# Kernel tuning notes

Hardware: AMD Instinct MI355X
Metric: run time of the kernel (lower is better)

## Reference

```python
import jax, jax.numpy as jnp
import numpy as np

EPS = 1e-9
NEG_BIG = -(2.0**32) + 1.0


def dice(x, alpha):
    # BN with center=False, scale=False at inference: moving_mean=0, moving_var=1
    x_norm = x * (1.0 / np.sqrt(1.0 + EPS)).astype(np.float32)
    p = jax.nn.sigmoid(x_norm)
    return alpha * (1.0 - p) * x + p * x


def setup_inputs() -> dict:
    key = jax.random.key(0)
    ks = jax.random.split(key, 12)
    B, T, D = 4096, 200, 128
    U = 128  # gru units == hidden_dim

    def glorot(k, shape):
        fan_in = shape[0]
        return (jax.random.normal(k, shape, dtype=jnp.float32) / np.sqrt(fan_in)).astype(jnp.float32)

    return {
        "interest_seq": jax.random.normal(ks[0], (B, T, D), dtype=jnp.float32),
        "target_emb": jax.random.normal(ks[1], (B, D), dtype=jnp.float32),
        "seq_length": jax.random.randint(ks[2], (B, 1), 0, T, dtype=jnp.int32),
        "W_att1": glorot(ks[3], (4 * D, 64)),
        "alpha1": jnp.zeros((64,), jnp.float32),
        "W_att2": glorot(ks[4], (64, 16)),
        "alpha2": jnp.zeros((16,), jnp.float32),
        "W_att3": glorot(ks[5], (16, 1)),
        "W_u": glorot(ks[6], (D + U, U)),
        "W_r": glorot(ks[7], (D + U, U)),
        "W_c": glorot(ks[8], (D + U, U)),
    }


def reference(interest_seq, target_emb, seq_length, W_att1, alpha1, W_att2, alpha2, W_att3, W_u, W_r, W_c):
    B, T, D = interest_seq.shape
    U = W_u.shape[1]

    # ---- Attention scores (return_score=True, sigmoid, no weight norm) ----
    q = jnp.broadcast_to(target_emb[:, None, :], (B, T, D))  # [B,T,D]
    k = interest_seq
    att_in = jnp.concatenate([q, k, q - k, q * k], axis=-1)  # [B,T,4D]
    h1 = dice(jnp.einsum('btf,fh->bth', att_in, W_att1), alpha1)
    h2 = dice(jnp.einsum('bth,hg->btg', h1, W_att2), alpha2)
    score = jnp.einsum('btg,go->bto', h2, W_att3)  # [B,T,1]

    valid = jnp.arange(T)[None, :] < seq_length  # [B,T] bool
    vmask = valid.astype(jnp.float32)[:, :, None]
    score = score * vmask + (1.0 - vmask) * NEG_BIG
    att = jax.nn.sigmoid(score)[:, :, 0]  # [B,T]

    # ---- AUGRU scan (return final hidden state) ----
    def step(h, xs):
        x_t, a_t, m_t = xs  # [B,D], [B], [B] bool
        gi = jnp.concatenate([x_t, h], axis=-1)  # [B, D+U]
        u = jax.nn.sigmoid(gi @ W_u)
        r = jax.nn.sigmoid(gi @ W_r)
        c = jnp.tanh(jnp.concatenate([x_t, r * h], axis=-1) @ W_c)
        u_t = u * a_t[:, None]
        h_new = (1.0 - u_t) * h + u_t * c
        h = jnp.where(m_t[:, None], h_new, h)
        return h, None

    xs = (jnp.swapaxes(interest_seq, 0, 1),  # [T,B,D]
          att.T,                              # [T,B]
          valid.T)                            # [T,B]
    h0 = jnp.zeros((B, U), dtype=interest_seq.dtype)
    h_final, _ = jax.lax.scan(step, h0, xs)
    return h_final
```

## Files before the change

kernel.cpp:

```cpp
#include <hip/hip_runtime.h>
#include <math.h>

typedef __bf16 bf16;
typedef __bf16 bf16x8 __attribute__((ext_vector_type(8)));
typedef float  f32x4  __attribute__((ext_vector_type(4)));

#define MFMA16(a,b,c) __builtin_amdgcn_mfma_f32_16x16x32_bf16((a),(b),(c),0,0,0)

#define B_SZ 4096
#define T_SZ 200
#define D_SZ 128
#define U_SZ 128
#define ACHUNK 4
#define AROWS 16

__device__ __forceinline__ float frcp_(float x) { return __builtin_amdgcn_rcpf(x); }
__device__ __forceinline__ float fsig(float x)  { return frcp_(1.0f + __expf(-x)); }
__device__ __forceinline__ float ftanh_(float x){ return 1.0f - 2.0f * frcp_(1.0f + __expf(2.0f * x)); }
__device__ __forceinline__ float dicef(float x, float alpha) {
    float p = fsig(x);
    return alpha * (1.0f - p) * x + p * x;
}
__device__ __forceinline__ void bar_lgkm() {
    asm volatile("s_waitcnt lgkmcnt(0)\n\ts_barrier" ::: "memory");
}

__global__ __launch_bounds__(256) void prep_kernel(
    const float* __restrict__ Q,
    const float* __restrict__ W1,
    const float* __restrict__ W2,
    float* __restrict__ BIAS,
    bf16*  __restrict__ W1P,
    bf16*  __restrict__ W2T)
{
    const int tid = threadIdx.x;
    if (blockIdx.x == 256) {
        #pragma unroll 4
        for (int it = 0; it < 64; ++it) {
            int idx = it * 256 + tid;
            int k = idx >> 6;
            int n = idx & 63;
            float v;
            if (k < 128) v = W1[(128 + k) * 64 + n] - W1[(256 + k) * 64 + n];
            else         v = W1[(384 + (k - 128)) * 64 + n];
            W1P[n * 256 + k] = (bf16)v;
        }
        #pragma unroll
        for (int it = 0; it < 4; ++it) {
            int idx = it * 256 + tid; int k = idx >> 4; int n = idx & 15;
            W2T[n * 64 + k] = (bf16)W2[k * 16 + n];
        }
        return;
    }
    const int b0   = blockIdx.x * 16;
    const int lane = tid & 63;
    const int w    = tid >> 6;
    const int quad = lane >> 4;
    const int l15  = lane & 15;

    bf16x8 a[4];
    #pragma unroll
    for (int kk = 0; kk < 4; ++kk) {
        const float* p = Q + (long)(b0 + l15) * D_SZ + kk * 32 + quad * 8;
        float4 x0 = ((const float4*)p)[0];
        float4 x1 = ((const float4*)p)[1];
        float xv[8] = {x0.x, x0.y, x0.z, x0.w, x1.x, x1.y, x1.z, x1.w};
        #pragma unroll
        for (int j = 0; j < 8; ++j) a[kk][j] = (bf16)xv[j];
    }
    const int n = w * 16 + l15;
    f32x4 acc = {};
    #pragma unroll
    for (int kk = 0; kk < 4; ++kk) {
        bf16x8 bf;
        #pragma unroll
        for (int j = 0; j < 8; ++j) {
            int k = kk * 32 + quad * 8 + j;
            bf[j] = (bf16)(W1[k * 64 + n] + W1[(256 + k) * 64 + n]);
        }
        acc = MFMA16(a[kk], bf, acc);
    }
    #pragma unroll
    for (int i = 0; i < 4; ++i)
        BIAS[(long)(b0 + quad * 4 + i) * 64 + n] = acc[i];
}

__global__ __launch_bounds__(512) void fused_kernel(
    const float* __restrict__ X,
    const float* __restrict__ Q,
    const int*   __restrict__ LEN,
    const float* __restrict__ A1,
    const float* __restrict__ A2g,
    const float* __restrict__ W3g,
    const float* __restrict__ BIAS,
    const bf16*  __restrict__ W1P,
    const bf16*  __restrict__ W2T,
    const float* __restrict__ WU,
    const float* __restrict__ WR,
    const float* __restrict__ WC,
    float* __restrict__ OUT)
{
    __shared__ bf16  Xs[2][ACHUNK][16][136];
    __shared__ bf16  XQs[ACHUNK][16][136];
    __shared__ bf16  W1s[64 * 264];
    __shared__ bf16  Hb[16][136];
    __shared__ bf16  RHb[16][136];
    __shared__ bf16  H1s[ACHUNK * 16 * 72];
    __shared__ float qf[16 * 132];
    __shared__ float bias_s[16 * 68];
    __shared__ float As[ACHUNK * 16];
    __shared__ int   lens16[16];

    const int tid  = threadIdx.x;
    const int lane = tid & 63;
    const int w    = tid >> 6;
    const int quad = lane >> 4;
    const int l15  = lane & 15;
    const int b0   = blockIdx.x * AROWS;
    const int n    = w * 16 + l15;

    for (int idx = tid; idx < 64 * 32; idx += 512) {
        int nn = idx >> 5, k8 = idx & 31;
        *(bf16x8*)&W1s[nn * 264 + k8 * 8] = *(const bf16x8*)(W1P + nn * 256 + k8 * 8);
    }
    for (int i = tid; i < 16 * 128; i += 512) {
        int r = i >> 7, k = i & 127;
        qf[r * 132 + k] = Q[(long)(b0 + r) * D_SZ + k];
    }
    for (int i = tid; i < 16 * 64; i += 512) {
        int r = i >> 6, c2 = i & 63;
        bias_s[r * 68 + c2] = BIAS[(long)(b0 + r) * 64 + c2];
    }
    if (tid < 16) lens16[tid] = LEN[b0 + tid];
    for (int i = tid; i < 16 * 136; i += 512) { ((bf16*)Hb)[i] = (bf16)0.f; ((bf16*)RHb)[i] = (bf16)0.f; }

    const float al1v = A1[(w & 3) * 16 + l15];
    const float al2v = A2g[l15];
    const float w3v  = W3g[l15];
    bf16x8 b2f[2];
    #pragma unroll
    for (int kk = 0; kk < 2; ++kk)
        b2f[kk] = *(const bf16x8*)(W2T + l15 * 64 + kk * 32 + quad * 8);

    bf16x8 Wf[3][2][4];
    {
        const float* Wg[3] = {WU, WR, WC};
        #pragma unroll
        for (int g = 0; g < 3; ++g)
            #pragma unroll
            for (int p = 0; p < 2; ++p)
                #pragma unroll
                for (int kk = 0; kk < 4; ++kk) {
                    #pragma unroll
                    for (int i = 0; i < 8; ++i) {
                        int k = p * 128 + kk * 32 + quad * 8 + i;
                        Wf[g][p][kk][i] = (bf16)Wg[g][k * 128 + n];
                    }
                }
    }

    float h[4] = {0.f, 0.f, 0.f, 0.f};

    float4 pf[4];
    auto issue_loads = [&](int c) {
        #pragma unroll
        for (int it = 0; it < 4; ++it) {
            int gidx = it * 512 + tid;
            int c4 = gidx & 31;
            int pair = gidx >> 5;
            int r = pair & 15;
            int s = pair >> 4;
            pf[it] = *(const float4*)(X + ((long)(b0 + r) * T_SZ + (c * ACHUNK + s)) * D_SZ + c4 * 4);
        }
    };
    auto commit_part = [&](int bufw, int it) {
        int gidx = it * 512 + tid;
        int c4 = gidx & 31;
        int pair = gidx >> 5;
        int r = pair & 15;
        int sl = pair >> 4;
        float4 v = pf[it];
        float4 qv = *(const float4*)&qf[r * 132 + c4 * 4];
        bf16* dx = &Xs[bufw][sl][r][c4 * 4];
        bf16* dq = &XQs[sl][r][c4 * 4];
        dx[0] = (bf16)v.x; dx[1] = (bf16)v.y; dx[2] = (bf16)v.z; dx[3] = (bf16)v.w;
        dq[0] = (bf16)(v.x * qv.x); dq[1] = (bf16)(v.y * qv.y);
        dq[2] = (bf16)(v.z * qv.z); dq[3] = (bf16)(v.w * qv.w);
    };
    auto xparts = [&](int bufw, int s, f32x4& pr_, f32x4& pu_, f32x4& pc_) {
        f32x4 r0 = {}, u0 = {}, c0 = {};
        #pragma unroll
        for (int kk = 0; kk < 4; ++kk) {
            bf16x8 ax = *(const bf16x8*)&Xs[bufw][s][l15][kk * 32 + quad * 8];
            r0 = MFMA16(ax, Wf[1][0][kk], r0);
            u0 = MFMA16(ax, Wf[0][0][kk], u0);
            c0 = MFMA16(ax, Wf[2][0][kk], c0);
        }
        pr_ = r0; pu_ = u0; pc_ = c0;
    };
    auto h1f = [&](int bufw, int s) {
        f32x4 acc = {};
        #pragma unroll
        for (int kk = 0; kk < 4; ++kk) {
            bf16x8 ax = *(const bf16x8*)&Xs[bufw][s][l15][kk * 32 + quad * 8];
            bf16x8 bw = *(const bf16x8*)&W1s[n * 264 + kk * 32 + quad * 8];
            acc = MFMA16(ax, bw, acc);
        }
        #pragma unroll
        for (int kk = 0; kk < 4; ++kk) {
            bf16x8 aq = *(const bf16x8*)&XQs[s][l15][kk * 32 + quad * 8];
            bf16x8 bw = *(const bf16x8*)&W1s[n * 264 + 128 + kk * 32 + quad * 8];
            acc = MFMA16(aq, bw, acc);
        }
        #pragma unroll
        for (int i = 0; i < 4; ++i) {
            int row = quad * 4 + i;
            float v = acc[i] + bias_s[row * 68 + n];
            H1s[(s * 16 + row) * 72 + n] = (bf16)dicef(v, al1v);
        }
    };
    auto h23f = [&](int s, int cc) {
        f32x4 acc2 = {};
        #pragma unroll
        for (int kk = 0; kk < 2; ++kk) {
            bf16x8 a2 = *(const bf16x8*)&H1s[(s * 16 + l15) * 72 + kk * 32 + quad * 8];
            acc2 = MFMA16(a2, b2f[kk], acc2);
        }
        float sv[4];
        #pragma unroll
        for (int i = 0; i < 4; ++i) sv[i] = dicef(acc2[i], al2v) * w3v;
        #pragma unroll
        for (int i = 0; i < 4; ++i) {
            sv[i] += __shfl_xor(sv[i], 1, 64);
            sv[i] += __shfl_xor(sv[i], 2, 64);
            sv[i] += __shfl_xor(sv[i], 4, 64);
            sv[i] += __shfl_xor(sv[i], 8, 64);
        }
        if (l15 == 0) {
            int t = cc * ACHUNK + s;
            #pragma unroll
            for (int i = 0; i < 4; ++i) {
                int row = quad * 4 + i;
                As[s * 16 + row] = (t < lens16[row]) ? fsig(sv[i]) : 0.0f;
            }
        }
    };

    issue_loads(0);
    __syncthreads();
    #pragma unroll
    for (int it = 0; it < 4; ++it) commit_part(0, it);
    bar_lgkm();
    if (w < 4) { h1f(0, 0); h1f(0, 1); h1f(0, 2); h1f(0, 3); }
    bar_lgkm();

    f32x4 pr, pu, pc;
    xparts(0, 0, pr, pu, pc);

    const int NCH = T_SZ / ACHUNK;
    for (int c = 0; c < NCH; ++c) {
        const int buf  = c & 1;
        const int bufN = buf ^ 1;
        if (c + 1 < NCH) issue_loads(c + 1);

        #pragma unroll
        for (int s = 0; s < ACHUNK; ++s) {
            bf16x8 ah[4];
            #pragma unroll
            for (int kk = 0; kk < 4; ++kk)
                ah[kk] = *(const bf16x8*)&Hb[l15][kk * 32 + quad * 8];
            #pragma unroll
            for (int kk = 0; kk < 4; ++kk) {
                pr = MFMA16(ah[kk], Wf[1][1][kk], pr);
                pu = MFMA16(ah[kk], Wf[0][1][kk], pu);
            }
            float uu[4];
            #pragma unroll
            for (int i = 0; i < 4; ++i) {
                float rr = fsig(pr[i]);
                RHb[quad * 4 + i][n] = (bf16)(rr * h[i]);
                uu[i] = fsig(pu[i]);
            }
            if (w >= 4) {
                if (w == 4 + s) h23f(s, c);
            } else if (s >= 1 && c + 1 < NCH) {
                h1f(bufN, s - 1);
            }
            bar_lgkm();
            bf16x8 ar[4];
            #pragma unroll
            for (int kk = 0; kk < 4; ++kk)
                ar[kk] = *(const bf16x8*)&RHb[l15][kk * 32 + quad * 8];
            #pragma unroll
            for (int kk = 0; kk < 4; ++kk)
                pc = MFMA16(ar[kk], Wf[2][1][kk], pc);
            f32x4 prN, puN, pcN;
            if (s + 1 < ACHUNK) xparts(buf, s + 1, prN, puN, pcN);
            #pragma unroll
            for (int i = 0; i < 4; ++i) {
                float a  = As[s * 16 + quad * 4 + i];
                float cg = ftanh_(pc[i]);
                float ut = uu[i] * a;
                float hn = (1.f - ut) * h[i] + ut * cg;
                h[i] = hn;
                Hb[quad * 4 + i][n] = (bf16)hn;
            }
            if (c + 1 < NCH) commit_part(bufN, s);
            bar_lgkm();
            if (s + 1 < ACHUNK) { pr = prN; pu = puN; pc = pcN; }
        }
        if (c + 1 < NCH) {
            xparts(bufN, 0, pr, pu, pc);
            if (w < 4) h1f(bufN, 3);
        }
    }

    #pragma unroll
    for (int i = 0; i < 4; ++i)
        OUT[(long)(b0 + quad * 4 + i) * U_SZ + n] = h[i];
}

extern "C" void kernel_launch(void* const* d_in, const int* in_sizes, int n_in,
                              void* d_out, int out_size, void* d_ws, size_t ws_size,
                              hipStream_t stream) {
    const float* X   = (const float*)d_in[0];
    const float* Q   = (const float*)d_in[1];
    const int*   LEN = (const int*)d_in[2];
    const float* W1  = (const float*)d_in[3];
    const float* A1  = (const float*)d_in[4];
    const float* W2  = (const float*)d_in[5];
    const float* A2  = (const float*)d_in[6];
    const float* W3  = (const float*)d_in[7];
    const float* WU  = (const float*)d_in[8];
    const float* WR  = (const float*)d_in[9];
    const float* WC  = (const float*)d_in[10];
    float* OUT = (float*)d_out;

    float* BIAS = (float*)d_ws;
    bf16*  W1P  = (bf16*)(BIAS + (size_t)B_SZ * 64);
    bf16*  W2T  = W1P + 64 * 256;

    prep_kernel<<<257, 256, 0, stream>>>(Q, W1, W2, BIAS, W1P, W2T);
    fused_kernel<<<B_SZ / AROWS, 512, 0, stream>>>(X, Q, LEN, A1, A2, W3,
                                                   BIAS, W1P, W2T, WU, WR, WC, OUT);
}
```

Measured before the change: 809.8 us.

## Split fused kernel into GRU waves and dedicated attention producer waves

The block grows from 8 to 12 waves. Eight waves run only the AUGRU recurrence. Four producer waves load X, convert it to bf16, compute the attention MLP and write scores into double-buffered As, staying in barrier lockstep with the GRU steps. The XQ shared buffer is dropped because producers keep x and x*q in registers, and s_setprio is raised around the MFMA sections. The aim is to take attention and load work off the recurrence critical path, at the cost of more registers per wave (launch bounds 768,3) and tight barrier coupling.

```diff
diff --git a/kernel.cpp b/kernel.cpp
--- a/kernel.cpp
+++ b/kernel.cpp
@@ -13,6 +13,7 @@
 #define U_SZ 128
 #define ACHUNK 4
 #define AROWS 16
+#define NCH (T_SZ / ACHUNK)
 
 __device__ __forceinline__ float frcp_(float x) { return __builtin_amdgcn_rcpf(x); }
 __device__ __forceinline__ float fsig(float x)  { return frcp_(1.0f + __expf(-x)); }
@@ -85,7 +86,7 @@
         BIAS[(long)(b0 + quad * 4 + i) * 64 + n] = acc[i];
 }
 
-__global__ __launch_bounds__(512) void fused_kernel(
+__global__ __launch_bounds__(768, 3) void fused_kernel(
     const float* __restrict__ X,
     const float* __restrict__ Q,
     const int*   __restrict__ LEN,
@@ -101,14 +102,13 @@
     float* __restrict__ OUT)
 {
     __shared__ bf16  Xs[2][ACHUNK][16][136];
-    __shared__ bf16  XQs[ACHUNK][16][136];
-    __shared__ bf16  W1s[64 * 264];
     __shared__ bf16  Hb[16][136];
     __shared__ bf16  RHb[16][136];
-    __shared__ bf16  H1s[ACHUNK * 16 * 72];
-    __shared__ float qf[16 * 132];
-    __shared__ float bias_s[16 * 68];
-    __shared__ float As[ACHUNK * 16];
+    __shared__ bf16  H1p[4][16][72];
+    __shared__ bf16  W1s[64][264];
+    __shared__ float qf[16][132];
+    __shared__ float bias_s[16][68];
+    __shared__ float As[2][64];
     __shared__ int   lens16[16];
 
     const int tid  = threadIdx.x;
@@ -117,207 +117,229 @@
     const int quad = lane >> 4;
     const int l15  = lane & 15;
     const int b0   = blockIdx.x * AROWS;
-    const int n    = w * 16 + l15;
-
-    for (int idx = tid; idx < 64 * 32; idx += 512) {
+
+    for (int idx = tid; idx < 64 * 32; idx += 768) {
         int nn = idx >> 5, k8 = idx & 31;
-        *(bf16x8*)&W1s[nn * 264 + k8 * 8] = *(const bf16x8*)(W1P + nn * 256 + k8 * 8);
-    }
-    for (int i = tid; i < 16 * 128; i += 512) {
+        *(bf16x8*)&W1s[nn][k8 * 8] = *(const bf16x8*)(W1P + nn * 256 + k8 * 8);
+    }
+    for (int i = tid; i < 16 * 128; i += 768) {
         int r = i >> 7, k = i & 127;
-        qf[r * 132 + k] = Q[(long)(b0 + r) * D_SZ + k];
-    }
-    for (int i = tid; i < 16 * 64; i += 512) {
-        int r = i >> 6, c2 = i & 63;
-        bias_s[r * 68 + c2] = BIAS[(long)(b0 + r) * 64 + c2];
+        qf[r][k] = Q[(long)(b0 + r) * D_SZ + k];
+    }
+    for (int i = tid; i < 16 * 64; i += 768) {
+        int r = i >> 6, cc = i & 63;
+        bias_s[r][cc] = BIAS[(long)(b0 + r) * 64 + cc];
     }
     if (tid < 16) lens16[tid] = LEN[b0 + tid];
-    for (int i = tid; i < 16 * 136; i += 512) { ((bf16*)Hb)[i] = (bf16)0.f; ((bf16*)RHb)[i] = (bf16)0.f; }
-
-    const float al1v = A1[(w & 3) * 16 + l15];
-    const float al2v = A2g[l15];
-    const float w3v  = W3g[l15];
-    bf16x8 b2f[2];
-    #pragma unroll
-    for (int kk = 0; kk < 2; ++kk)
-        b2f[kk] = *(const bf16x8*)(W2T + l15 * 64 + kk * 32 + quad * 8);
-
-    bf16x8 Wf[3][2][4];
-    {
-        const float* Wg[3] = {WU, WR, WC};
-        #pragma unroll
-        for (int g = 0; g < 3; ++g)
-            #pragma unroll
-            for (int p = 0; p < 2; ++p)
+    for (int i = tid; i < 16 * 136; i += 768) {
+        ((bf16*)Hb)[i] = (bf16)0.f; ((bf16*)RHb)[i] = (bf16)0.f;
+    }
+    __syncthreads();
+
+    if (w < 8) {
+        const int n = w * 16 + l15;
+        bf16x8 Wf[3][2][4];
+        {
+            const float* Wg[3] = {WU, WR, WC};
+            #pragma unroll
+            for (int g = 0; g < 3; ++g)
+                #pragma unroll
+                for (int p = 0; p < 2; ++p)
+                    #pragma unroll
+                    for (int kk = 0; kk < 4; ++kk) {
+                        #pragma unroll
+                        for (int i = 0; i < 8; ++i) {
+                            int k = p * 128 + kk * 32 + quad * 8 + i;
+                            Wf[g][p][kk][i] = (bf16)Wg[g][k * 128 + n];
+                        }
+                    }
+        }
+        float h[4] = {0.f, 0.f, 0.f, 0.f};
+        f32x4 pr, pu, pc;
+        auto xparts = [&](int bufw, int s) {
+            f32x4 r0 = {}, u0 = {}, c0 = {};
+            __builtin_amdgcn_s_setprio(1);
+            #pragma unroll
+            for (int kk = 0; kk < 4; ++kk) {
+                bf16x8 ax = *(const bf16x8*)&Xs[bufw][s][l15][kk * 32 + quad * 8];
+                r0 = MFMA16(ax, Wf[1][0][kk], r0);
+                u0 = MFMA16(ax, Wf[0][0][kk], u0);
+                c0 = MFMA16(ax, Wf[2][0][kk], c0);
+            }
+            __builtin_amdgcn_s_setprio(0);
+            pr = r0; pu = u0; pc = c0;
+        };
+
+        bar_lgkm();
+        xparts(0, 0);
+
+        for (int c = 0; c < NCH; ++c) {
+            const int buf  = c & 1;
+            const int bufN = buf ^ 1;
+            #pragma unroll
+            for (int s = 0; s < ACHUNK; ++s) {
+                bf16x8 ah[4];
+                #pragma unroll
+                for (int kk = 0; kk < 4; ++kk)
+                    ah[kk] = *(const bf16x8*)&Hb[l15][kk * 32 + quad * 8];
+                __builtin_amdgcn_s_setprio(1);
                 #pragma unroll
                 for (int kk = 0; kk < 4; ++kk) {
-                    #pragma unroll
-                    for (int i = 0; i < 8; ++i) {
-                        int k = p * 128 + kk * 32 + quad * 8 + i;
-                        Wf[g][p][kk][i] = (bf16)Wg[g][k * 128 + n];
-                    }
-                }
-    }
-
-    float h[4] = {0.f, 0.f, 0.f, 0.f};
-
-    float4 pf[4];
-    auto issue_loads = [&](int c) {
-        #pragma unroll
-        for (int it = 0; it < 4; ++it) {
-            int gidx = it * 512 + tid;
-            int c4 = gidx & 31;
-            int pair = gidx >> 5;
-            int r = pair & 15;
-            int s = pair >> 4;
-            pf[it] = *(const float4*)(X + ((long)(b0 + r) * T_SZ + (c * ACHUNK + s)) * D_SZ + c4 * 4);
-        }
-    };
-    auto commit_part = [&](int bufw, int it) {
-        int gidx = it * 512 + tid;
-        int c4 = gidx & 31;
-        int pair = gidx >> 5;
-        int r = pair & 15;
-        int sl = pair >> 4;
-        float4 v = pf[it];
-        float4 qv = *(const float4*)&qf[r * 132 + c4 * 4];
-        bf16* dx = &Xs[bufw][sl][r][c4 * 4];
-        bf16* dq = &XQs[sl][r][c4 * 4];
-        dx[0] = (bf16)v.x; dx[1] = (bf16)v.y; dx[2] = (bf16)v.z; dx[3] = (bf16)v.w;
-        dq[0] = (bf16)(v.x * qv.x); dq[1] = (bf16)(v.y * qv.y);
-        dq[2] = (bf16)(v.z * qv.z); dq[3] = (bf16)(v.w * qv.w);
-    };
-    auto xparts = [&](int bufw, int s, f32x4& pr_, f32x4& pu_, f32x4& pc_) {
-        f32x4 r0 = {}, u0 = {}, c0 = {};
-        #pragma unroll
-        for (int kk = 0; kk < 4; ++kk) {
-            bf16x8 ax = *(const bf16x8*)&Xs[bufw][s][l15][kk * 32 + quad * 8];
-            r0 = MFMA16(ax, Wf[1][0][kk], r0);
-            u0 = MFMA16(ax, Wf[0][0][kk], u0);
-            c0 = MFMA16(ax, Wf[2][0][kk], c0);
-        }
-        pr_ = r0; pu_ = u0; pc_ = c0;
-    };
-    auto h1f = [&](int bufw, int s) {
-        f32x4 acc = {};
-        #pragma unroll
-        for (int kk = 0; kk < 4; ++kk) {
-            bf16x8 ax = *(const bf16x8*)&Xs[bufw][s][l15][kk * 32 + quad * 8];
-            bf16x8 bw = *(const bf16x8*)&W1s[n * 264 + kk * 32 + quad * 8];
-            acc = MFMA16(ax, bw, acc);
-        }
-        #pragma unroll
-        for (int kk = 0; kk < 4; ++kk) {
-            bf16x8 aq = *(const bf16x8*)&XQs[s][l15][kk * 32 + quad * 8];
-            bf16x8 bw = *(const bf16x8*)&W1s[n * 264 + 128 + kk * 32 + quad * 8];
-            acc = MFMA16(aq, bw, acc);
-        }
-        #pragma unroll
-        for (int i = 0; i < 4; ++i) {
-            int row = quad * 4 + i;
-            float v = acc[i] + bias_s[row * 68 + n];
-            H1s[(s * 16 + row) * 72 + n] = (bf16)dicef(v, al1v);
-        }
-    };
-    auto h23f = [&](int s, int cc) {
-        f32x4 acc2 = {};
-        #pragma unroll
-        for (int kk = 0; kk < 2; ++kk) {
-            bf16x8 a2 = *(const bf16x8*)&H1s[(s * 16 + l15) * 72 + kk * 32 + quad * 8];
-            acc2 = MFMA16(a2, b2f[kk], acc2);
-        }
-        float sv[4];
-        #pragma unroll
-        for (int i = 0; i < 4; ++i) sv[i] = dicef(acc2[i], al2v) * w3v;
-        #pragma unroll
-        for (int i = 0; i < 4; ++i) {
-            sv[i] += __shfl_xor(sv[i], 1, 64);
-            sv[i] += __shfl_xor(sv[i], 2, 64);
-            sv[i] += __shfl_xor(sv[i], 4, 64);
-            sv[i] += __shfl_xor(sv[i], 8, 64);
-        }
-        if (l15 == 0) {
-            int t = cc * ACHUNK + s;
+                    pr = MFMA16(ah[kk], Wf[1][1][kk], pr);
+                    pu = MFMA16(ah[kk], Wf[0][1][kk], pu);
+                }
+                __builtin_amdgcn_s_setprio(0);
+                float uu[4];
+                #pragma unroll
+                for (int i = 0; i < 4; ++i) {
+                    float rr = fsig(pr[i]);
+                    RHb[quad * 4 + i][n] = (bf16)(rr * h[i]);
+                    uu[i] = fsig(pu[i]);
+                }
+                bar_lgkm();
+                bf16x8 ar[4];
+                #pragma unroll
+                for (int kk = 0; kk < 4; ++kk)
+                    ar[kk] = *(const bf16x8*)&RHb[l15][kk * 32 + quad * 8];
+                __builtin_amdgcn_s_setprio(1);
+                #pragma unroll
+                for (int kk = 0; kk < 4; ++kk)
+                    pc = MFMA16(ar[kk], Wf[2][1][kk], pc);
+                __builtin_amdgcn_s_setprio(0);
+                #pragma unroll
+                for (int i = 0; i < 4; ++i) {
+                    float a  = As[buf][s * 16 + quad * 4 + i];
+                    float cg = ftanh_(pc[i]);
+                    float ut = uu[i] * a;
+                    float hn = (1.f - ut) * h[i] + ut * cg;
+                    h[i] = hn;
+                    Hb[quad * 4 + i][n] = (bf16)hn;
+                }
+                if (s + 1 < ACHUNK)      xparts(buf, s + 1);
+                else if (c + 1 < NCH)    xparts(bufN, 0);
+                bar_lgkm();
+            }
+        }
+        #pragma unroll
+        for (int i = 0; i < 4; ++i)
+            OUT[(long)(b0 + quad * 4 + i) * U_SZ + n] = h[i];
+    } else {
+        const int pw = w - 8;
+        float al1r[4];
+        #pragma unroll
+        for (int nt = 0; nt < 4; ++nt) al1r[nt] = A1[nt * 16 + l15];
+        const float al2v = A2g[l15];
+        const float w3v  = W3g[l15];
+        bf16x8 b2f[2];
+        #pragma unroll
+        for (int kk = 0; kk < 2; ++kk)
+            b2f[kk] = *(const bf16x8*)(W2T + l15 * 64 + kk * 32 + quad * 8);
+
+        float4 pf[8];
+        bf16x8 axp[4], aqp[4];
+
+        auto p_issue = [&](int cn) {
+            const float* xp = X + ((long)(b0 + l15) * T_SZ + cn * ACHUNK + pw) * D_SZ;
+            #pragma unroll
+            for (int kk = 0; kk < 4; ++kk) {
+                const float* p = xp + kk * 32 + quad * 8;
+                pf[kk * 2]     = ((const float4*)p)[0];
+                pf[kk * 2 + 1] = ((const float4*)p)[1];
+            }
+        };
+        auto p_convert = [&]() {
+            #pragma unroll
+            for (int kk = 0; kk < 4; ++kk) {
+                float4 xa = pf[kk * 2], xb = pf[kk * 2 + 1];
+                float xv[8] = {xa.x, xa.y, xa.z, xa.w, xb.x, xb.y, xb.z, xb.w};
+                const float* qp = &qf[l15][kk * 32 + quad * 8];
+                #pragma unroll
+                for (int j = 0; j < 8; ++j) {
+                    axp[kk][j] = (bf16)xv[j];
+                    aqp[kk][j] = (bf16)(xv[j] * qp[j]);
+                }
+            }
+        };
+        auto p_writeXs = [&](int xb) {
+            #pragma unroll
+            for (int kk = 0; kk < 4; ++kk)
+                *(bf16x8*)&Xs[xb][pw][l15][kk * 32 + quad * 8] = axp[kk];
+        };
+        auto p_h1 = [&](int nt) {
+            f32x4 acc = {};
+            #pragma unroll
+            for (int kk = 0; kk < 4; ++kk) {
+                bf16x8 bw = *(const bf16x8*)&W1s[nt * 16 + l15][kk * 32 + quad * 8];
+                acc = MFMA16(axp[kk], bw, acc);
+            }
+            #pragma unroll
+            for (int kk = 0; kk < 4; ++kk) {
+                bf16x8 bw = *(const bf16x8*)&W1s[nt * 16 + l15][128 + kk * 32 + quad * 8];
+                acc = MFMA16(aqp[kk], bw, acc);
+            }
             #pragma unroll
             for (int i = 0; i < 4; ++i) {
                 int row = quad * 4 + i;
-                As[s * 16 + row] = (t < lens16[row]) ? fsig(sv[i]) : 0.0f;
-            }
-        }
-    };
-
-    issue_loads(0);
-    __syncthreads();
-    #pragma unroll
-    for (int it = 0; it < 4; ++it) commit_part(0, it);
-    bar_lgkm();
-    if (w < 4) { h1f(0, 0); h1f(0, 1); h1f(0, 2); h1f(0, 3); }
-    bar_lgkm();
-
-    f32x4 pr, pu, pc;
-    xparts(0, 0, pr, pu, pc);
-
-    const int NCH = T_SZ / ACHUNK;
-    for (int c = 0; c < NCH; ++c) {
-        const int buf  = c & 1;
-        const int bufN = buf ^ 1;
-        if (c + 1 < NCH) issue_loads(c + 1);
-
-        #pragma unroll
-        for (int s = 0; s < ACHUNK; ++s) {
-            bf16x8 ah[4];
-            #pragma unroll
-            for (int kk = 0; kk < 4; ++kk)
-                ah[kk] = *(const bf16x8*)&Hb[l15][kk * 32 + quad * 8];
-            #pragma unroll
-            for (int kk = 0; kk < 4; ++kk) {
-                pr = MFMA16(ah[kk], Wf[1][1][kk], pr);
-                pu = MFMA16(ah[kk], Wf[0][1][kk], pu);
-            }
-            float uu[4];
+                float v = acc[i] + bias_s[row][nt * 16 + l15];
+                H1p[pw][row][nt * 16 + l15] = (bf16)dicef(v, al1r[nt]);
+            }
+        };
+        auto p_h23 = [&](int cn, int ab) {
+            f32x4 acc2 = {};
+            #pragma unroll
+            for (int kk = 0; kk < 2; ++kk) {
+                bf16x8 a2 = *(const bf16x8*)&H1p[pw][l15][kk * 32 + quad * 8];
+                acc2 = MFMA16(a2, b2f[kk], acc2);
+            }
+            float sv[4];
+            #pragma unroll
+            for (int i = 0; i < 4; ++i) sv[i] = dicef(acc2[i], al2v) * w3v;
             #pragma unroll
             for (int i = 0; i < 4; ++i) {
-                float rr = fsig(pr[i]);
-                RHb[quad * 4 + i][n] = (bf16)(rr * h[i]);
-                uu[i] = fsig(pu[i]);
-            }
-            if (w >= 4) {
-                if (w == 4 + s) h23f(s, c);
-            } else if (s >= 1 && c + 1 < NCH) {
-                h1f(bufN, s - 1);
-            }
-            bar_lgkm();
-            bf16x8 ar[4];
-            #pragma unroll
-            for (int kk = 0; kk < 4; ++kk)
-                ar[kk] = *(const bf16x8*)&RHb[l15][kk * 32 + quad * 8];
-            #pragma unroll
-            for (int kk = 0; kk < 4; ++kk)
-                pc = MFMA16(ar[kk], Wf[2][1][kk], pc);
-            f32x4 prN, puN, pcN;
-            if (s + 1 < ACHUNK) xparts(buf, s + 1, prN, puN, pcN);
-            #pragma unroll
-            for (int i = 0; i < 4; ++i) {
-                float a  = As[s * 16 + quad * 4 + i];
-                float cg = ftanh_(pc[i]);
-                float ut = uu[i] * a;
-                float hn = (1.f - ut) * h[i] + ut * cg;
-                h[i] = hn;
-                Hb[quad * 4 + i][n] = (bf16)hn;
-            }
-            if (c + 1 < NCH) commit_part(bufN, s);
-            bar_lgkm();
-            if (s + 1 < ACHUNK) { pr = prN; pu = puN; pc = pcN; }
-        }
-        if (c + 1 < NCH) {
-            xparts(bufN, 0, pr, pu, pc);
-            if (w < 4) h1f(bufN, 3);
-        }
-    }
-
-    #pragma unroll
-    for (int i = 0; i < 4; ++i)
-        OUT[(long)(b0 + quad * 4 + i) * U_SZ + n] = h[i];
+                sv[i] += __shfl_xor(sv[i], 1, 64);
+                sv[i] += __shfl_xor(sv[i], 2, 64);
+                sv[i] += __shfl_xor(sv[i], 4, 64);
+                sv[i] += __shfl_xor(sv[i], 8, 64);
+            }
+            if (l15 == 0) {
+                int t = cn * ACHUNK + pw;
+                #pragma unroll
+                for (int i = 0; i < 4; ++i) {
+                    int row = quad * 4 + i;
+                    As[ab][pw * 16 + row] = (t < lens16[row]) ? fsig(sv[i]) : 0.0f;
+                }
+            }
+        };
+
+        p_issue(0);
+        p_convert();
+        p_writeXs(0);
+        p_h1(0); p_h1(1); p_h1(2); p_h1(3);
+        p_h23(0, 0);
+        if (NCH > 1) p_issue(1);
+        bar_lgkm();
+
+        for (int c = 0; c < NCH; ++c) {
+            const int cn = c + 1;
+            const int xb = cn & 1;
+            const bool act = cn < NCH;
+            if (act) { p_convert(); p_writeXs(xb); }
+            bar_lgkm();
+            if (c + 2 < NCH) p_issue(c + 2);
+            bar_lgkm();
+            if (act) p_h1(0);
+            bar_lgkm();
+            if (act) p_h1(1);
+            bar_lgkm();
+            if (act) p_h1(2);
+            bar_lgkm();
+            if (act) p_h1(3);
+            bar_lgkm();
+            if (act) p_h23(cn, xb);
+            bar_lgkm();
+            bar_lgkm();
+        }
+    }
 }
 
 extern "C" void kernel_launch(void* const* d_in, const int* in_sizes, int n_in,
@@ -341,6 +363,6 @@
     bf16*  W2T  = W1P + 64 * 256;
 
     prep_kernel<<<257, 256, 0, stream>>>(Q, W1, W2, BIAS, W1P, W2T);
-    fused_kernel<<<B_SZ / AROWS, 512, 0, stream>>>(X, Q, LEN, A1, A2, W3,
+    fused_kernel<<<B_SZ / AROWS, 768, 0, stream>>>(X, Q, LEN, A1, A2, W3,
                                                    BIAS, W1P, W2T, WU, WR, WC, OUT);
 }
```

Result: faster. 715.4 us (-11.7%).
